# Performance work log

Hardware: AMD Instinct MI355X
Metric: run time of the kernel (lower is better)

The kernel has to match this reference:

```python
import jax, jax.numpy as jnp
import numpy as np

N_NODES = 207
N_EDGES = 1722
N_SLOTS = 288  # 288 / resolution with resolution = 1


def setup_inputs() -> dict:
    key = jax.random.key(0)
    ks = jax.random.split(key, 7)
    B, C, L = 1024, 2, 64
    inputs = jax.random.normal(ks[0], (B, C, N_NODES, L), dtype=jnp.float32)
    weight_diff = jax.random.normal(ks[1], (N_SLOTS, N_EDGES), dtype=jnp.float32) / 1000.0
    bias_diffusion = jax.random.normal(ks[2], (N_SLOTS, N_NODES), dtype=jnp.float32) / 10.0
    weight_self_loop = jax.random.normal(ks[3], (N_SLOTS, N_NODES), dtype=jnp.float32) / 10.0
    ind = jax.random.randint(ks[4], (B,), 0, N_SLOTS, dtype=jnp.int32)
    edge_i = jax.random.randint(ks[5], (N_EDGES,), 0, N_NODES, dtype=jnp.int32)
    edge_j = jax.random.randint(ks[6], (N_EDGES,), 0, N_NODES, dtype=jnp.int32)
    return {"inputs": inputs, "weight_diff": weight_diff,
            "bias_diffusion": bias_diffusion, "weight_self_loop": weight_self_loop,
            "ind": ind, "edge_i": edge_i, "edge_j": edge_j}


def reference(inputs, weight_diff, bias_diffusion, weight_self_loop, ind, edge_i, edge_j):
    # resolution = 1 -> slot index ii == ind
    x = inputs[:, 0, :, :]                      # [B, N, L]
    B, N, _ = x.shape
    w = weight_diff[ind]                        # [B, E] per-sample edge weights
    # symmetric scatter into batched dense adjacency (duplicates sum, as in sparse_coo_tensor)
    A = jnp.zeros((B, N, N), dtype=x.dtype)
    A = A.at[:, edge_i, edge_j].add(w).at[:, edge_j, edge_i].add(w)
    deg = jnp.sum(A, axis=1)                    # [B, N]  (sum over dim 1, as in torch code)
    lap = deg[:, :, None] * jnp.eye(N, dtype=x.dtype) - A  # L = diag(deg) - A
    diffusion = jnp.einsum('nvl,nwv->nwl', x, lap) + bias_diffusion[ind][:, :, None]
    self_loop = weight_self_loop[ind][:, :, None] * x
    return diffusion + x + self_loop
```

## Files before the change

kernel.cpp:

```cpp
#include <hip/hip_runtime.h>

#define N_NODES 207
#define N_EDGES 1722
#define N_SLOTS 288
#define L_DIM   64

__device__ __forceinline__ unsigned int f2bf_rtn_bits_hi(float f) {
    unsigned int u = __float_as_uint(f);
    unsigned int r = u + 0x7FFFu + ((u >> 16) & 1u);
    return r & 0xFFFF0000u;
}

__global__ __launch_bounds__(256) void build_csr_kernel(
    const int* __restrict__ edge_i, const int* __restrict__ edge_j,
    int* __restrict__ row_start, unsigned int* __restrict__ csr_packed) {
    __shared__ int cnt[N_NODES];
    __shared__ int rs[N_NODES + 1];
    const int tid = threadIdx.x;

    for (int n = tid; n < N_NODES; n += 256) cnt[n] = 0;
    __syncthreads();
    for (int e = tid; e < N_EDGES; e += 256) {
        atomicAdd(&cnt[edge_i[e]], 1);
        atomicAdd(&cnt[edge_j[e]], 1);
    }
    __syncthreads();
    if (tid == 0) {
        int acc = 0;
        for (int n = 0; n < N_NODES; ++n) { rs[n] = acc; acc += cnt[n]; }
        rs[N_NODES] = acc;
    }
    __syncthreads();
    for (int n = tid; n <= N_NODES; n += 256) row_start[n] = rs[n];
    for (int n = tid; n < N_NODES; n += 256) cnt[n] = rs[n];
    __syncthreads();
    for (int e = tid; e < N_EDGES; e += 256) {
        const unsigned int i = edge_i[e], j = edge_j[e];
        const unsigned int ep = ((unsigned int)e) << 8;
        int p = atomicAdd(&cnt[i], 1);
        csr_packed[p] = ep | j;
        int q = atomicAdd(&cnt[j], 1);
        csr_packed[q] = ep | i;
    }
}

__global__ __launch_bounds__(256) void coef_kernel(
    const float* __restrict__ weight_diff, const float* __restrict__ bias_diffusion,
    const float* __restrict__ weight_self_loop,
    const int* __restrict__ row_start, const unsigned int* __restrict__ csr_packed,
    float2* __restrict__ coefbias) {
    __shared__ float wrow[N_EDGES];
    const int s = blockIdx.x;
    for (int e = threadIdx.x; e < N_EDGES; e += 256)
        wrow[e] = weight_diff[(size_t)s * N_EDGES + e];
    __syncthreads();
    const int n = threadIdx.x;
    if (n < N_NODES) {
        float d = 0.f;
        const int e0 = row_start[n], e1 = row_start[n + 1];
        for (int k = e0; k < e1; ++k) d += wrow[csr_packed[k] >> 8];
        coefbias[s * N_NODES + n] = make_float2(
            1.f + weight_self_loop[s * N_NODES + n] + d,
            bias_diffusion[s * N_NODES + n]);
    }
}

__global__ __launch_bounds__(512, 8) void diffusion_gcn_kernel(
    const float* __restrict__ inputs,
    const float* __restrict__ weight_diff,
    const int*   __restrict__ ind,
    const int*   __restrict__ row_start,
    const unsigned int* __restrict__ csr_packed,
    const float2* __restrict__ coefbias,
    float* __restrict__ out) {
    __shared__ unsigned short xs[N_NODES * L_DIM];
    __shared__ unsigned int   wnb[2 * N_EDGES];
    __shared__ unsigned short rs[N_NODES + 1];

    const int b    = blockIdx.x;
    const int tid  = threadIdx.x;
    const int slot = ind[b];

    const float* xb = inputs + (size_t)b * (2 * N_NODES * L_DIM);

    const float4* xb4 = (const float4*)xb;
    for (int k = tid; k < (N_NODES * L_DIM) / 4; k += 512) {
        const float4 v = xb4[k];
        const unsigned int lo = (f2bf_rtn_bits_hi(v.x) >> 16) | f2bf_rtn_bits_hi(v.y);
        const unsigned int hi = (f2bf_rtn_bits_hi(v.z) >> 16) | f2bf_rtn_bits_hi(v.w);
        ((uint2*)xs)[k] = make_uint2(lo, hi);
    }
    const float* wrow = weight_diff + (size_t)slot * N_EDGES;
    for (int k = tid; k < 2 * N_EDGES; k += 512) {
        const unsigned int c = csr_packed[k];
        wnb[k] = f2bf_rtn_bits_hi(wrow[c >> 8]) | (c & 255u);
    }
    for (int n = tid; n <= N_NODES; n += 512) rs[n] = (unsigned short)row_start[n];
    __syncthreads();

    const int lane = tid & 63;
    const int wv   = tid >> 6;
    float* ob = out + (size_t)b * (N_NODES * L_DIM);

    for (int n = wv; n < N_NODES; n += 8) {
        const int e0 = rs[n], e1 = rs[n + 1];
        float s = 0.f;
        #pragma unroll 4
        for (int k = e0; k < e1; ++k) {
            const unsigned int p = wnb[k];
            const float w  = __uint_as_float(p & 0xFFFF0000u);
            const float xv = __uint_as_float(
                (unsigned int)xs[(p & 255u) * L_DIM + lane] << 16);
            s = fmaf(w, xv, s);
        }
        const float2 cb = coefbias[slot * N_NODES + n];
        const float  xg = xb[n * L_DIM + lane];
        ob[n * L_DIM + lane] = fmaf(cb.x, xg, cb.y) - s;
    }
}

extern "C" void kernel_launch(void* const* d_in, const int* in_sizes, int n_in,
                              void* d_out, int out_size, void* d_ws, size_t ws_size,
                              hipStream_t stream) {
    const float* inputs           = (const float*)d_in[0];
    const float* weight_diff      = (const float*)d_in[1];
    const float* bias_diffusion   = (const float*)d_in[2];
    const float* weight_self_loop = (const float*)d_in[3];
    const int*   ind              = (const int*)d_in[4];
    const int*   edge_i           = (const int*)d_in[5];
    const int*   edge_j           = (const int*)d_in[6];
    float* out = (float*)d_out;

    const int B = in_sizes[4];

    int*          row_start  = (int*)d_ws;
    unsigned int* csr_packed = (unsigned int*)((char*)d_ws + 832);
    float2*       coefbias   = (float2*)((char*)d_ws + 14608);

    build_csr_kernel<<<1, 256, 0, stream>>>(edge_i, edge_j, row_start, csr_packed);
    coef_kernel<<<N_SLOTS, 256, 0, stream>>>(
        weight_diff, bias_diffusion, weight_self_loop, row_start, csr_packed, coefbias);
    diffusion_gcn_kernel<<<B, 512, 0, stream>>>(
        inputs, weight_diff, ind, row_start, csr_packed, coefbias, out);
}
```

Baseline: 237.9 us.

## Replace sparse CSR diffusion with per-slot dense operator and bf16 MFMA GEMM

```diff
diff --git a/kernel.cpp b/kernel.cpp
--- a/kernel.cpp
+++ b/kernel.cpp
@@ -1,40 +1,159 @@
 #include <hip/hip_runtime.h>
 
-#define N_NODES 207
-#define N_EDGES 1722
-#define N_SLOTS 288
-#define L_DIM   64
-
-__device__ __forceinline__ unsigned int f2bf_rtn_bits_hi(float f) {
+#define NN 207
+#define NE 1722
+#define NS 288
+#define LDIM 64
+#define KSTEPS 7
+#define RT_TILES 13
+#define XT_RS 232
+
+typedef short bf16x8 __attribute__((ext_vector_type(8)));
+typedef float f32x4  __attribute__((ext_vector_type(4)));
+
+__device__ __forceinline__ unsigned int f2bf(float f) {
     unsigned int u = __float_as_uint(f);
-    unsigned int r = u + 0x7FFFu + ((u >> 16) & 1u);
-    return r & 0xFFFF0000u;
+    return (u + 0x7FFFu + ((u >> 16) & 1u)) >> 16;
+}
+
+
+__global__ __launch_bounds__(256) void build_m_kernel(
+    const float* __restrict__ wd,
+    const float* __restrict__ wsl,
+    const int* __restrict__ ei, const int* __restrict__ ej,
+    unsigned int* __restrict__ fragbuf) {
+    __shared__ float M[64 * 224];
+    __shared__ float deg[NN];
+    const int sb = blockIdx.x;
+    const int s = sb >> 2, p = sb & 3;
+    const int r0 = p * 64;
+    const int t = threadIdx.x;
+
+    for (int i = t; i < 64 * 224; i += 256) M[i] = 0.f;
+    for (int n = t; n < NN; n += 256) deg[n] = 0.f;
+    __syncthreads();
+
+    const float* wrow = wd + (size_t)s * NE;
+    for (int e = t; e < NE; e += 256) {
+        const float w = wrow[e];
+        const int i = ei[e], j = ej[e];
+        atomicAdd(&deg[i], w);
+        atomicAdd(&deg[j], w);
+        const int ri = i - r0;
+        if (ri >= 0 && ri < 64) atomicAdd(&M[ri * 224 + j], -w);
+        const int rj = j - r0;
+        if (rj >= 0 && rj < 64) atomicAdd(&M[rj * 224 + i], -w);
+    }
+    __syncthreads();
+    if (t < 64) {
+        const int n = r0 + t;
+        if (n < NN) M[t * 224 + n] += 1.f + wsl[(size_t)s * NN + n] + deg[n];
+    }
+    __syncthreads();
+
+    const int ntiles = (p < 3) ? 4 : 1;
+    for (int it = 0; it < ntiles * KSTEPS; ++it) {
+        const int rtl = it / KSTEPS, ks = it % KSTEPS;
+        const int rt = p * 4 + rtl;
+        const int lane = t >> 2, pr = t & 3;
+        const int row = rtl * 16 + (lane & 15);
+        const int k = ks * 32 + (lane >> 4) * 8 + pr * 2;
+        const unsigned int v = f2bf(M[row * 224 + k]) |
+                               (f2bf(M[row * 224 + k + 1]) << 16);
+        fragbuf[(((size_t)s * RT_TILES + rt) * KSTEPS + ks) * 256 + t] = v;
+    }
+}
+
+__global__ __launch_bounds__(256, 4) void gemm_kernel(
+    const float* __restrict__ inputs,
+    const float* __restrict__ bias_d,
+    const int*   __restrict__ ind,
+    const unsigned int* __restrict__ fragbuf,
+    float* __restrict__ out) {
+    __shared__ __align__(16) unsigned short xT[LDIM * XT_RS];
+
+    const int b = blockIdx.x, t = threadIdx.x;
+    const int s = ind[b];
+    const float* xb = inputs + (size_t)b * (2 * NN * LDIM);
+
+    for (int it = t; it < 112 * 64; it += 256) {
+        const int n = it & 63, kp = it >> 6;
+        unsigned int v = 0;
+        if (kp < 103) {
+            v = f2bf(xb[(2 * kp) * 64 + n]) | (f2bf(xb[(2 * kp + 1) * 64 + n]) << 16);
+        } else if (kp == 103) {
+            v = f2bf(xb[206 * 64 + n]);
+        }
+        *(unsigned int*)&xT[n * XT_RS + kp * 2] = v;
+    }
+    __syncthreads();
+
+    const int lane = t & 63, wv = t >> 6;
+    const int quad = lane >> 4, m16 = lane & 15;
+
+    bf16x8 Bf[KSTEPS];
+    #pragma unroll
+    for (int ks = 0; ks < KSTEPS; ++ks)
+        Bf[ks] = *(const bf16x8*)&xT[(wv * 16 + m16) * XT_RS + ks * 32 + quad * 8];
+
+    const bf16x8* Ab = ((const bf16x8*)fragbuf) +
+                       (size_t)s * RT_TILES * KSTEPS * 64 + lane;
+    float* ob = out + (size_t)b * NN * LDIM + wv * 16 + m16;
+    const float* bias_row = bias_d + (size_t)s * NN;
+
+    bf16x8 A0[KSTEPS], A1[KSTEPS];
+    #pragma unroll
+    for (int ks = 0; ks < KSTEPS; ++ks) A0[ks] = Ab[ks * 64];
+
+    #pragma unroll
+    for (int rt = 0; rt < RT_TILES; ++rt) {
+        const bf16x8* Acur = (rt & 1) ? A1 : A0;
+        bf16x8*       Anxt = (rt & 1) ? A0 : A1;
+        if (rt + 1 < RT_TILES) {
+            const bf16x8* An = Ab + (size_t)(rt + 1) * KSTEPS * 64;
+            #pragma unroll
+            for (int ks = 0; ks < KSTEPS; ++ks) Anxt[ks] = An[ks * 64];
+        }
+        f32x4 acc = {0.f, 0.f, 0.f, 0.f};
+        #pragma unroll
+        for (int ks = 0; ks < KSTEPS; ++ks)
+            acc = __builtin_amdgcn_mfma_f32_16x16x32_bf16(Acur[ks], Bf[ks], acc, 0, 0, 0);
+        #pragma unroll
+        for (int r = 0; r < 4; ++r) {
+            const int node = rt * 16 + quad * 4 + r;
+            if (node < NN) ob[(size_t)node * 64] = acc[r] + bias_row[node];
+        }
+    }
+}
+
+__device__ __forceinline__ unsigned int f2bf_hi(float f) {
+    unsigned int u = __float_as_uint(f);
+    return (u + 0x7FFFu + ((u >> 16) & 1u)) & 0xFFFF0000u;
 }
 
 __global__ __launch_bounds__(256) void build_csr_kernel(
     const int* __restrict__ edge_i, const int* __restrict__ edge_j,
     int* __restrict__ row_start, unsigned int* __restrict__ csr_packed) {
-    __shared__ int cnt[N_NODES];
-    __shared__ int rs[N_NODES + 1];
+    __shared__ int cnt[NN];
+    __shared__ int rs[NN + 1];
     const int tid = threadIdx.x;
-
-    for (int n = tid; n < N_NODES; n += 256) cnt[n] = 0;
-    __syncthreads();
-    for (int e = tid; e < N_EDGES; e += 256) {
+    for (int n = tid; n < NN; n += 256) cnt[n] = 0;
+    __syncthreads();
+    for (int e = tid; e < NE; e += 256) {
         atomicAdd(&cnt[edge_i[e]], 1);
         atomicAdd(&cnt[edge_j[e]], 1);
     }
     __syncthreads();
     if (tid == 0) {
         int acc = 0;
-        for (int n = 0; n < N_NODES; ++n) { rs[n] = acc; acc += cnt[n]; }
-        rs[N_NODES] = acc;
-    }
-    __syncthreads();
-    for (int n = tid; n <= N_NODES; n += 256) row_start[n] = rs[n];
-    for (int n = tid; n < N_NODES; n += 256) cnt[n] = rs[n];
-    __syncthreads();
-    for (int e = tid; e < N_EDGES; e += 256) {
+        for (int n = 0; n < NN; ++n) { rs[n] = acc; acc += cnt[n]; }
+        rs[NN] = acc;
+    }
+    __syncthreads();
+    for (int n = tid; n <= NN; n += 256) row_start[n] = rs[n];
+    for (int n = tid; n < NN; n += 256) cnt[n] = rs[n];
+    __syncthreads();
+    for (int e = tid; e < NE; e += 256) {
         const unsigned int i = edge_i[e], j = edge_j[e];
         const unsigned int ep = ((unsigned int)e) << 8;
         int p = atomicAdd(&cnt[i], 1);
@@ -49,73 +168,61 @@
     const float* __restrict__ weight_self_loop,
     const int* __restrict__ row_start, const unsigned int* __restrict__ csr_packed,
     float2* __restrict__ coefbias) {
-    __shared__ float wrow[N_EDGES];
+    __shared__ float wrow[NE];
     const int s = blockIdx.x;
-    for (int e = threadIdx.x; e < N_EDGES; e += 256)
-        wrow[e] = weight_diff[(size_t)s * N_EDGES + e];
+    for (int e = threadIdx.x; e < NE; e += 256)
+        wrow[e] = weight_diff[(size_t)s * NE + e];
     __syncthreads();
     const int n = threadIdx.x;
-    if (n < N_NODES) {
+    if (n < NN) {
         float d = 0.f;
         const int e0 = row_start[n], e1 = row_start[n + 1];
         for (int k = e0; k < e1; ++k) d += wrow[csr_packed[k] >> 8];
-        coefbias[s * N_NODES + n] = make_float2(
-            1.f + weight_self_loop[s * N_NODES + n] + d,
-            bias_diffusion[s * N_NODES + n]);
+        coefbias[s * NN + n] = make_float2(
+            1.f + weight_self_loop[s * NN + n] + d, bias_diffusion[s * NN + n]);
     }
 }
 
 __global__ __launch_bounds__(512, 8) void diffusion_gcn_kernel(
-    const float* __restrict__ inputs,
-    const float* __restrict__ weight_diff,
-    const int*   __restrict__ ind,
-    const int*   __restrict__ row_start,
+    const float* __restrict__ inputs, const float* __restrict__ weight_diff,
+    const int* __restrict__ ind, const int* __restrict__ row_start,
     const unsigned int* __restrict__ csr_packed,
-    const float2* __restrict__ coefbias,
-    float* __restrict__ out) {
-    __shared__ unsigned short xs[N_NODES * L_DIM];
-    __shared__ unsigned int   wnb[2 * N_EDGES];
-    __shared__ unsigned short rs[N_NODES + 1];
-
-    const int b    = blockIdx.x;
-    const int tid  = threadIdx.x;
+    const float2* __restrict__ coefbias, float* __restrict__ out) {
+    __shared__ unsigned short xs[NN * LDIM];
+    __shared__ unsigned int   wnb[2 * NE];
+    __shared__ unsigned short rs[NN + 1];
+    const int b = blockIdx.x, tid = threadIdx.x;
     const int slot = ind[b];
-
-    const float* xb = inputs + (size_t)b * (2 * N_NODES * L_DIM);
-
+    const float* xb = inputs + (size_t)b * (2 * NN * LDIM);
     const float4* xb4 = (const float4*)xb;
-    for (int k = tid; k < (N_NODES * L_DIM) / 4; k += 512) {
+    for (int k = tid; k < (NN * LDIM) / 4; k += 512) {
         const float4 v = xb4[k];
-        const unsigned int lo = (f2bf_rtn_bits_hi(v.x) >> 16) | f2bf_rtn_bits_hi(v.y);
-        const unsigned int hi = (f2bf_rtn_bits_hi(v.z) >> 16) | f2bf_rtn_bits_hi(v.w);
+        const unsigned int lo = (f2bf_hi(v.x) >> 16) | f2bf_hi(v.y);
+        const unsigned int hi = (f2bf_hi(v.z) >> 16) | f2bf_hi(v.w);
         ((uint2*)xs)[k] = make_uint2(lo, hi);
     }
-    const float* wrow = weight_diff + (size_t)slot * N_EDGES;
-    for (int k = tid; k < 2 * N_EDGES; k += 512) {
+    const float* wrow = weight_diff + (size_t)slot * NE;
+    for (int k = tid; k < 2 * NE; k += 512) {
         const unsigned int c = csr_packed[k];
-        wnb[k] = f2bf_rtn_bits_hi(wrow[c >> 8]) | (c & 255u);
-    }
-    for (int n = tid; n <= N_NODES; n += 512) rs[n] = (unsigned short)row_start[n];
-    __syncthreads();
-
-    const int lane = tid & 63;
-    const int wv   = tid >> 6;
-    float* ob = out + (size_t)b * (N_NODES * L_DIM);
-
-    for (int n = wv; n < N_NODES; n += 8) {
+        wnb[k] = f2bf_hi(wrow[c >> 8]) | (c & 255u);
+    }
+    for (int n = tid; n <= NN; n += 512) rs[n] = (unsigned short)row_start[n];
+    __syncthreads();
+    const int lane = tid & 63, wv = tid >> 6;
+    float* ob = out + (size_t)b * (NN * LDIM);
+    for (int n = wv; n < NN; n += 8) {
         const int e0 = rs[n], e1 = rs[n + 1];
         float s = 0.f;
         #pragma unroll 4
         for (int k = e0; k < e1; ++k) {
             const unsigned int p = wnb[k];
-            const float w  = __uint_as_float(p & 0xFFFF0000u);
-            const float xv = __uint_as_float(
-                (unsigned int)xs[(p & 255u) * L_DIM + lane] << 16);
+            const float w = __uint_as_float(p & 0xFFFF0000u);
+            const float xv = __uint_as_float((unsigned int)xs[(p & 255u) * LDIM + lane] << 16);
             s = fmaf(w, xv, s);
         }
-        const float2 cb = coefbias[slot * N_NODES + n];
-        const float  xg = xb[n * L_DIM + lane];
-        ob[n * L_DIM + lane] = fmaf(cb.x, xg, cb.y) - s;
+        const float2 cb = coefbias[slot * NN + n];
+        const float xg = xb[n * LDIM + lane];
+        ob[n * LDIM + lane] = fmaf(cb.x, xg, cb.y) - s;
     }
 }
 
@@ -130,16 +237,24 @@
     const int*   edge_i           = (const int*)d_in[5];
     const int*   edge_j           = (const int*)d_in[6];
     float* out = (float*)d_out;
-
     const int B = in_sizes[4];
 
-    int*          row_start  = (int*)d_ws;
-    unsigned int* csr_packed = (unsigned int*)((char*)d_ws + 832);
-    float2*       coefbias   = (float2*)((char*)d_ws + 14608);
-
-    build_csr_kernel<<<1, 256, 0, stream>>>(edge_i, edge_j, row_start, csr_packed);
-    coef_kernel<<<N_SLOTS, 256, 0, stream>>>(
-        weight_diff, bias_diffusion, weight_self_loop, row_start, csr_packed, coefbias);
-    diffusion_gcn_kernel<<<B, 512, 0, stream>>>(
-        inputs, weight_diff, ind, row_start, csr_packed, coefbias, out);
-}
+    const size_t FRAG_BYTES = (size_t)NS * RT_TILES * KSTEPS * 1024;
+
+    if (ws_size >= FRAG_BYTES) {
+        unsigned int* fragbuf = (unsigned int*)d_ws;
+        build_m_kernel<<<NS * 4, 256, 0, stream>>>(
+            weight_diff, weight_self_loop, edge_i, edge_j, fragbuf);
+        gemm_kernel<<<B, 256, 0, stream>>>(
+            inputs, bias_diffusion, ind, fragbuf, out);
+    } else {
+        int*          row_start  = (int*)d_ws;
+        unsigned int* csr_packed = (unsigned int*)((char*)d_ws + 832);
+        float2*       coefbias   = (float2*)((char*)d_ws + 14608);
+        build_csr_kernel<<<1, 256, 0, stream>>>(edge_i, edge_j, row_start, csr_packed);
+        coef_kernel<<<NS, 256, 0, stream>>>(
+            weight_diff, bias_diffusion, weight_self_loop, row_start, csr_packed, coefbias);
+        diffusion_gcn_kernel<<<B, 512, 0, stream>>>(
+            inputs, weight_diff, ind, row_start, csr_packed, coefbias, out);
+    }
+}
```

After: 240.3 us. About the same (+1.0%).
